# Kernel tuning notes

Measured on AMD Instinct MI355X. Metric: run time of the kernel, lower is better.

## Reference

```python
import jax, jax.numpy as jnp
import numpy as np

B, S, E, N = 2, 2048, 768, 12
H = E // N

def setup_inputs() -> dict:
    key = jax.random.key(0)
    k1, k2, k3, k4, k5 = jax.random.split(key, 5)
    x = jax.random.normal(k1, (B, S, E), dtype=jnp.float32)
    Wqkv = jax.random.normal(k2, (E, 3 * E), dtype=jnp.float32) * (1.0 / np.sqrt(E))
    bqkv = jax.random.normal(k3, (3 * E,), dtype=jnp.float32) * 0.02
    Wproj = jax.random.normal(k4, (E, E), dtype=jnp.float32) * (1.0 / np.sqrt(E))
    bproj = jax.random.normal(k5, (E,), dtype=jnp.float32) * 0.02
    mask = jnp.tril(jnp.ones((S, S), dtype=jnp.int32))[None, None]  # (1,1,S,S) causal
    return {"mask": mask, "x": x, "Wqkv": Wqkv, "bqkv": bqkv, "Wproj": Wproj, "bproj": bproj}

def reference(mask, x, Wqkv, bqkv, Wproj, bproj):
    Bx, Sx, Ex = x.shape
    Hd = Ex // N
    qkv = x @ Wqkv + bqkv                       # (B,S,3E)
    q, k, v = jnp.split(qkv, 3, axis=-1)
    q = q.reshape(Bx, Sx, N, Hd).transpose(0, 2, 1, 3)  # (B,N,S,H)
    k = k.reshape(Bx, Sx, N, Hd).transpose(0, 2, 1, 3)
    v = v.reshape(Bx, Sx, N, Hd).transpose(0, 2, 1, 3)
    att = jnp.einsum('bnsh,bnth->bnst', q, k) / jnp.sqrt(jnp.float32(Hd))
    att = jnp.where(mask == 0, -jnp.inf, att)   # causal masked_fill
    p = jax.nn.softmax(att, axis=-1)            # dropout p=0.0 -> identity
    y = jnp.einsum('bnst,bnth->bnsh', p, v)     # (B,N,S,H)
    y = y.transpose(0, 2, 1, 3).reshape(Bx, Sx, Ex)
    return y @ Wproj + bproj
```

## Files before the change

kernel.cpp:

```cpp
#include <hip/hip_runtime.h>
#include <hip/hip_bf16.h>
#include <math.h>

#define S_LEN 2048
#define E_DIM 768
#define NHEAD 12
#define HDIM 64
#define BATCH 2
#define MROWS (BATCH * S_LEN)
#define KDIM E_DIM
#define NBN (BATCH * NHEAD)
#define NTASKS 768

#define QSCALE 0.1803368801111204f
#define REF2   11.541560327111707f

typedef __attribute__((ext_vector_type(8))) short bf16x8;
typedef __attribute__((ext_vector_type(4))) float f32x4;

__device__ inline float exp2_fast(float x) {
    return __builtin_amdgcn_exp2f(x);
}

__device__ inline unsigned short f2bf(float f) {
    __hip_bfloat16 h = __float2bfloat16(f);
    union { __hip_bfloat16 b; unsigned short u; } v; v.b = h;
    return v.u;
}

__global__ __launch_bounds__(256) void prep(
    const float* __restrict__ x, unsigned short* __restrict__ Xb,
    const float* __restrict__ Wqkv, unsigned short* __restrict__ WqkvT,
    const float* __restrict__ Wproj, unsigned short* __restrict__ WprojT)
{
    __shared__ float t[32][33];
    const int blk = blockIdx.x, tid = threadIdx.x;
    if (blk < 3072) {
        const int i = blk * 256 + tid;
        const float4 a = ((const float4*)x)[i];
        ushort4 o;
        o.x = f2bf(a.x); o.y = f2bf(a.y); o.z = f2bf(a.z); o.w = f2bf(a.w);
        ((ushort4*)Xb)[i] = o;
        return;
    }
    const float* W; unsigned short* WT; int N, bt;
    if (blk < 3072 + 1728) { bt = blk - 3072; N = 3 * E_DIM; W = Wqkv; WT = WqkvT; }
    else                   { bt = blk - 4800; N = E_DIM;     W = Wproj; WT = WprojT; }
    const int bx = bt % (N / 32), by = bt / (N / 32);
    const int k0 = by * 32, n0 = bx * 32;
    const int r = tid >> 3, c4 = (tid & 7) * 4;
    const float4 v = *(const float4*)&W[(size_t)(k0 + r) * N + n0 + c4];
    t[r][c4 + 0] = v.x; t[r][c4 + 1] = v.y; t[r][c4 + 2] = v.z; t[r][c4 + 3] = v.w;
    __syncthreads();
    ushort4 o;
    o.x = f2bf(t[c4 + 0][r]); o.y = f2bf(t[c4 + 1][r]);
    o.z = f2bf(t[c4 + 2][r]); o.w = f2bf(t[c4 + 3][r]);
    *(ushort4*)&WT[(size_t)(n0 + r) * KDIM + k0 + c4] = o;
}

template <int EPI, int BM, int BN>
__global__ __launch_bounds__(256, 3) void gemm_t(
    const unsigned short* __restrict__ A, const unsigned short* __restrict__ BT,
    const float* __restrict__ bias, void* __restrict__ out0,
    void* __restrict__ out1, void* __restrict__ out2, int Nn)
{
    constexpr int MF = BM / 32;
    constexpr int NF = BN / 32;
    __shared__ unsigned short As[BM * 64];
    __shared__ unsigned short Bs[BN * 64];
    const int tid = threadIdx.x;
    const int lane = tid & 63;
    const int wid = tid >> 6;
    const int lr = lane & 15, lg = lane >> 4;
    const int wr = wid >> 1, wc = wid & 1;
    const int m0 = blockIdx.y * BM;
    const int n0 = blockIdx.x * BN;
    const int srow = lane >> 3, scol = (lane & 7) * 8;

    f32x4 acc[MF][NF];
    #pragma unroll
    for (int i = 0; i < MF; ++i)
        #pragma unroll
        for (int j = 0; j < NF; ++j) acc[i][j] = (f32x4){0.f, 0.f, 0.f, 0.f};

    for (int k0 = 0; k0 < KDIM; k0 += 64) {
        __syncthreads();
        #pragma unroll
        for (int c = 0; c < MF; ++c) {
            const int chunk = wid * MF + c;
            const int row = chunk * 8 + srow;
            const unsigned short* ga = A + (size_t)(m0 + row) * KDIM + k0 + scol;
            __builtin_amdgcn_global_load_lds(
                (const __attribute__((address_space(1))) void*)ga,
                (__attribute__((address_space(3))) void*)&As[chunk * 512], 16, 0, 0);
        }
        #pragma unroll
        for (int c = 0; c < NF; ++c) {
            const int chunk = wid * NF + c;
            const int row = chunk * 8 + srow;
            const unsigned short* gb = BT + (size_t)(n0 + row) * KDIM + k0 + scol;
            __builtin_amdgcn_global_load_lds(
                (const __attribute__((address_space(1))) void*)gb,
                (__attribute__((address_space(3))) void*)&Bs[chunk * 512], 16, 0, 0);
        }
        __syncthreads();

        #pragma unroll
        for (int kk = 0; kk < 2; ++kk) {
            bf16x8 af[MF], bf[NF];
            #pragma unroll
            for (int mt = 0; mt < MF; ++mt)
                af[mt] = *(const bf16x8*)&As[(wr * (BM / 2) + mt * 16 + lr) * 64 + kk * 32 + lg * 8];
            #pragma unroll
            for (int nt = 0; nt < NF; ++nt)
                bf[nt] = *(const bf16x8*)&Bs[(wc * (BN / 2) + nt * 16 + lr) * 64 + kk * 32 + lg * 8];
            #pragma unroll
            for (int mt = 0; mt < MF; ++mt)
                #pragma unroll
                for (int nt = 0; nt < NF; ++nt)
                    acc[mt][nt] = __builtin_amdgcn_mfma_f32_16x16x32_bf16(
                        af[mt], bf[nt], acc[mt][nt], 0, 0, 0);
        }
    }

    #pragma unroll
    for (int mt = 0; mt < MF; ++mt) {
        const int rowbase = m0 + wr * (BM / 2) + mt * 16 + lg * 4;
        #pragma unroll
        for (int nt = 0; nt < NF; ++nt) {
            const int col = n0 + wc * (BN / 2) + nt * 16 + lr;
            if (EPI == 0) {
                float* O = (float*)out0;
                const float bv = bias[col];
                #pragma unroll
                for (int r = 0; r < 4; ++r)
                    O[(size_t)(rowbase + r) * Nn + col] = acc[mt][nt][r] + bv;
            } else {
                const int which = col / E_DIM;
                const int rem = col % E_DIM;
                const int head = rem >> 6, h = rem & 63;
                const float bv = bias[col];
                if (which == 2) {
                    const int b = rowbase >> 11, s0 = rowbase & (S_LEN - 1);
                    const int scolv = (s0 & ~63) | ((s0 & 63) ^ ((h & 7) << 3));
                    unsigned short* VT = (unsigned short*)out2;
                    ushort4 pk;
                    pk.x = f2bf(acc[mt][nt][0] + bv);
                    pk.y = f2bf(acc[mt][nt][1] + bv);
                    pk.z = f2bf(acc[mt][nt][2] + bv);
                    pk.w = f2bf(acc[mt][nt][3] + bv);
                    *(ushort4*)&VT[((size_t)(b * NHEAD + head) * HDIM + h) * S_LEN + scolv] = pk;
                } else {
                    unsigned short* dst = (which == 0) ? (unsigned short*)out0
                                                       : (unsigned short*)out1;
                    const float sc = (which == 0) ? QSCALE : 1.0f;
                    #pragma unroll
                    for (int r = 0; r < 4; ++r) {
                        const int m = rowbase + r;
                        const int b = m >> 11, s = m & (S_LEN - 1);
                        const int hh = (which == 1) ? (h ^ ((s & 7) << 3)) : h;
                        dst[(((size_t)(b * NHEAD + head) * S_LEN) + s) * HDIM + hh] =
                            f2bf((acc[mt][nt][r] + bv) * sc);
                    }
                }
            }
        }
    }
}

__global__ __launch_bounds__(256, 4) void attn_mfma(
    const unsigned short* __restrict__ Qb, const unsigned short* __restrict__ Kb,
    const unsigned short* __restrict__ VTb, unsigned short* __restrict__ Y,
    float* __restrict__ ws_o, float* __restrict__ ws_l)
{
    __shared__ unsigned short smem[5 * 4096];

    const int tid = threadIdx.x;
    const int lane = tid & 63;
    const int wid = tid >> 6;
    const int lr = lane & 15;
    const int lg = lane >> 4;

    unsigned short* const Pw = smem + 16384 + wid * 1024;

    const short one_bf = (short)0x3F80;
    bf16x8 onesB;
    #pragma unroll
    for (int j = 0; j < 8; ++j) onesB[j] = one_bf;

    const int B = blockIdx.x;
    const int xcd = B & 7, slot = B >> 3;
    const int bn = xcd + (slot >> 5) * 8;
    const int rest = slot & 31;
    const int jj = rest & 15, half = rest >> 4;
    const int b = bn / NHEAD, n = bn % NHEAD;

    const unsigned short* Kg = Kb + (size_t)bn * S_LEN * HDIM;
    const unsigned short* Vg = VTb + (size_t)bn * HDIM * S_LEN;

    auto run_pass = [&](int qb, int t0, int t1, int mode) {
        const size_t qoff = ((size_t)bn * S_LEN + (qb * 64 + wid * 16 + lr)) * HDIM;
        const bf16x8 qB0 = *(const bf16x8*)(Qb + qoff + lg * 8);
        const bf16x8 qB1 = *(const bf16x8*)(Qb + qoff + 32 + lg * 8);

        f32x4 o[4];
        #pragma unroll
        for (int ht = 0; ht < 4; ++ht) o[ht] = (f32x4){0.f, 0.f, 0.f, 0.f};
        f32x4 lsum = (f32x4){0.f, 0.f, 0.f, 0.f};

        __syncthreads();
        #pragma unroll
        for (int e = 0; e < 2; ++e) {
            const int chunk = wid * 2 + e;
            __builtin_amdgcn_global_load_lds(
                (const __attribute__((address_space(1))) void*)
                    (Kg + (size_t)t0 * 4096 + chunk * 512 + lane * 8),
                (__attribute__((address_space(3))) void*)&smem[chunk * 512], 16, 0, 0);
            __builtin_amdgcn_global_load_lds(
                (const __attribute__((address_space(1))) void*)
                    (Vg + (size_t)(chunk * 8 + (lane >> 3)) * S_LEN + t0 * 64 + (lane & 7) * 8),
                (__attribute__((address_space(3))) void*)&smem[8192 + chunk * 512], 16, 0, 0);
        }

        int cur = 0;
        for (int t = t0; t < t1; ++t) {
            __syncthreads();
            if (t + 1 < t1) {
                #pragma unroll
                for (int e = 0; e < 2; ++e) {
                    const int chunk = wid * 2 + e;
                    __builtin_amdgcn_global_load_lds(
                        (const __attribute__((address_space(1))) void*)
                            (Kg + (size_t)(t + 1) * 4096 + chunk * 512 + lane * 8),
                        (__attribute__((address_space(3))) void*)
                            &smem[(cur ^ 1) * 4096 + chunk * 512], 16, 0, 0);
                    __builtin_amdgcn_global_load_lds(
                        (const __attribute__((address_space(1))) void*)
                            (Vg + (size_t)(chunk * 8 + (lane >> 3)) * S_LEN + (t + 1) * 64
                                + (lane & 7) * 8),
                        (__attribute__((address_space(3))) void*)
                            &smem[8192 + (cur ^ 1) * 4096 + chunk * 512], 16, 0, 0);
                }
            }

            const unsigned short* Kc = smem + cur * 4096;
            const unsigned short* Vc = smem + 8192 + cur * 4096;

            f32x4 s[4];
            __builtin_amdgcn_s_setprio(1);
            #pragma unroll
            for (int ct = 0; ct < 4; ++ct) {
                const int kr = ct * 16 + lr;
                const int xo = (kr & 7) << 3;
                const bf16x8 kb0 = *(const bf16x8*)&Kc[kr * 64 + ((lg * 8) ^ xo)];
                const bf16x8 kb1 = *(const bf16x8*)&Kc[kr * 64 + ((32 + lg * 8) ^ xo)];
                f32x4 a = (f32x4){0.f, 0.f, 0.f, 0.f};
                a = __builtin_amdgcn_mfma_f32_16x16x32_bf16(kb0, qB0, a, 0, 0, 0);
                a = __builtin_amdgcn_mfma_f32_16x16x32_bf16(kb1, qB1, a, 0, 0, 0);
                s[ct] = a;
            }
            __builtin_amdgcn_s_setprio(0);

            if (t == qb) {
                const int q = qb * 64 + wid * 16 + lr;
                #pragma unroll
                for (int ct = 0; ct < 4; ++ct) {
                    #pragma unroll
                    for (int r = 0; r < 4; ++r) {
                        const int k = t * 64 + ct * 16 + lg * 4 + r;
                        if (k > q) s[ct][r] = -1e30f;
                    }
                }
            }

            const int pxo = (lr & 7) << 3;
            #pragma unroll
            for (int ct = 0; ct < 4; ++ct) {
                const float p0 = exp2_fast(s[ct][0] - REF2);
                const float p1 = exp2_fast(s[ct][1] - REF2);
                const float p2 = exp2_fast(s[ct][2] - REF2);
                const float p3 = exp2_fast(s[ct][3] - REF2);
                ushort4 pk;
                pk.x = f2bf(p0); pk.y = f2bf(p1); pk.z = f2bf(p2); pk.w = f2bf(p3);
                *(ushort4*)&Pw[lr * 64 + ((ct * 16 + lg * 4) ^ pxo)] = pk;
            }

            const bf16x8 pa0 = *(const bf16x8*)&Pw[lr * 64 + ((lg * 8) ^ pxo)];
            const bf16x8 pa1 = *(const bf16x8*)&Pw[lr * 64 + ((32 + lg * 8) ^ pxo)];
            __builtin_amdgcn_s_setprio(1);
            lsum = __builtin_amdgcn_mfma_f32_16x16x32_bf16(pa0, onesB, lsum, 0, 0, 0);
            lsum = __builtin_amdgcn_mfma_f32_16x16x32_bf16(pa1, onesB, lsum, 0, 0, 0);
            #pragma unroll
            for (int ht = 0; ht < 4; ++ht) {
                const int h = ht * 16 + lr;
                const int xo = (h & 7) << 3;
                const bf16x8 vb0 = *(const bf16x8*)&Vc[h * 64 + ((lg * 8) ^ xo)];
                const bf16x8 vb1 = *(const bf16x8*)&Vc[h * 64 + ((32 + lg * 8) ^ xo)];
                o[ht] = __builtin_amdgcn_mfma_f32_16x16x32_bf16(pa0, vb0, o[ht], 0, 0, 0);
                o[ht] = __builtin_amdgcn_mfma_f32_16x16x32_bf16(pa1, vb1, o[ht], 0, 0, 0);
            }
            __builtin_amdgcn_s_setprio(0);
            cur ^= 1;
        }

        if (mode == 2) {
            float invl[4];
            #pragma unroll
            for (int r = 0; r < 4; ++r) invl[r] = 1.f / lsum[r];
            #pragma unroll
            for (int r = 0; r < 4; ++r) {
                const int qrow = qb * 64 + wid * 16 + lg * 4 + r;
                unsigned short* yrow =
                    Y + ((size_t)(b * S_LEN + qrow)) * E_DIM + n * HDIM;
                #pragma unroll
                for (int ht = 0; ht < 4; ++ht)
                    yrow[ht * 16 + lr] = f2bf(o[ht][r] * invl[r]);
            }
        } else {
            const size_t m = (size_t)(bn * 16 + (qb - 16)) * 2 + mode;
            float* wo = ws_o + m * 4096;
            const int rowl = wid * 16 + lg * 4;
            #pragma unroll
            for (int ht = 0; ht < 4; ++ht)
                #pragma unroll
                for (int r = 0; r < 4; ++r)
                    wo[(rowl + r) * 64 + ht * 16 + lr] = o[ht][r];
            if (lr == 0) {
                #pragma unroll
                for (int r = 0; r < 4; ++r)
                    ws_l[m * 64 + rowl + r] = lsum[r];
            }
        }
    };

    if (half == 0) {
        run_pass(31 - jj, 0, 16, 0);
    } else {
        run_pass(31 - jj, 16, 32 - jj, 1);
        run_pass(jj, 0, jj + 1, 2);
    }
}

__global__ __launch_bounds__(256) void attn_merge(
    const float* __restrict__ ws_o, const float* __restrict__ ws_l,
    unsigned short* __restrict__ Y)
{
    const int m = blockIdx.x;
    const int bn = m / 16, qb = 16 + (m % 16);
    const int b = bn / NHEAD, n = bn % NHEAD;
    const int tid = threadIdx.x;
    const int r = tid >> 2, h0 = (tid & 3) * 16;

    const float* o0 = ws_o + ((size_t)m * 2 + 0) * 4096 + r * 64 + h0;
    const float* o1 = ws_o + ((size_t)m * 2 + 1) * 4096 + r * 64 + h0;
    const float l = ws_l[((size_t)m * 2 + 0) * 64 + r] +
                    ws_l[((size_t)m * 2 + 1) * 64 + r];
    const float inv = 1.f / l;
    unsigned short* yrow =
        Y + ((size_t)(b * S_LEN + qb * 64 + r)) * E_DIM + n * HDIM + h0;
    #pragma unroll
    for (int q = 0; q < 16; q += 4) {
        const float4 a = *(const float4*)(o0 + q);
        const float4 c = *(const float4*)(o1 + q);
        ushort4 pk;
        pk.x = f2bf((a.x + c.x) * inv); pk.y = f2bf((a.y + c.y) * inv);
        pk.z = f2bf((a.z + c.z) * inv); pk.w = f2bf((a.w + c.w) * inv);
        *(ushort4*)&yrow[q] = pk;
    }
}

extern "C" void kernel_launch(void* const* d_in, const int* in_sizes, int n_in,
                              void* d_out, int out_size, void* d_ws, size_t ws_size,
                              hipStream_t stream) {
    const float* x     = (const float*)d_in[1];
    const float* Wqkv  = (const float*)d_in[2];
    const float* bqkv  = (const float*)d_in[3];
    const float* Wproj = (const float*)d_in[4];
    const float* bproj = (const float*)d_in[5];
    float* out = (float*)d_out;

    const size_t per = (size_t)BATCH * NHEAD * S_LEN * HDIM;
    unsigned short* Xb     = (unsigned short*)d_ws;
    unsigned short* WqkvT  = Xb + (size_t)MROWS * E_DIM;
    unsigned short* WprojT = WqkvT + (size_t)3 * E_DIM * E_DIM;
    unsigned short* Qb     = WprojT + (size_t)E_DIM * E_DIM;
    unsigned short* Kb     = Qb + per;
    unsigned short* VTb    = Kb + per;
    unsigned short* Yb     = VTb + per;
    float*          ws_o   = (float*)(Yb + (size_t)MROWS * E_DIM);
    float*          ws_l   = ws_o + (size_t)384 * 2 * 4096;

    prep<<<5376, 256, 0, stream>>>(x, Xb, Wqkv, WqkvT, Wproj, WprojT);
    gemm_t<1, 128, 96><<<dim3(3 * E_DIM / 96, MROWS / 128), 256, 0, stream>>>(
        Xb, WqkvT, bqkv, Qb, Kb, VTb, 3 * E_DIM);
    attn_mfma<<<NTASKS, 256, 0, stream>>>(Qb, Kb, VTb, Yb, ws_o, ws_l);
    attn_merge<<<384, 256, 0, stream>>>(ws_o, ws_l, Yb);
    gemm_t<0, 64, 64><<<dim3(E_DIM / 64, MROWS / 64), 256, 0, stream>>>(
        Yb, WprojT, bproj, out, nullptr, nullptr, E_DIM);
}
```

Baseline: 78.61 us.

## Double-buffer GEMM LDS staging with K=32 tiles; store split-attention partials in bf16

The GEMM mainloop now uses two LDS buffers with 32-wide K tiles. The next tile's global-to-LDS load is issued before computing on the current one, and one barrier per iteration is dropped. The hope is to overlap memory latency with MFMA work, at the cost of twice as many loop iterations with half the work each. Separately, the split-attention partial outputs are stored as bf16 instead of fp32, which halves workspace traffic for the merge kernel at some accuracy cost.

After: 82.23 us. 1.05x slower.

```diff
diff --git a/kernel.cpp b/kernel.cpp
--- a/kernel.cpp
+++ b/kernel.cpp
@@ -26,6 +26,11 @@
     __hip_bfloat16 h = __float2bfloat16(f);
     union { __hip_bfloat16 b; unsigned short u; } v; v.b = h;
     return v.u;
+}
+
+__device__ inline float bf2f(unsigned short u) {
+    union { unsigned u32; float f; } v; v.u32 = ((unsigned)u) << 16;
+    return v.f;
 }
 
 __global__ __launch_bounds__(256) void prep(
@@ -66,8 +71,10 @@
 {
     constexpr int MF = BM / 32;
     constexpr int NF = BN / 32;
-    __shared__ unsigned short As[BM * 64];
-    __shared__ unsigned short Bs[BN * 64];
+    constexpr int ACH = BM / 16;
+    constexpr int BCH = BN / 16;
+    __shared__ unsigned short As[2][BM * 32];
+    __shared__ unsigned short Bs[2][BN * 32];
     const int tid = threadIdx.x;
     const int lane = tid & 63;
     const int wid = tid >> 6;
@@ -75,7 +82,7 @@
     const int wr = wid >> 1, wc = wid & 1;
     const int m0 = blockIdx.y * BM;
     const int n0 = blockIdx.x * BN;
-    const int srow = lane >> 3, scol = (lane & 7) * 8;
+    const int crow = lane >> 2, ccol = (lane & 3) * 8;
 
     f32x4 acc[MF][NF];
     #pragma unroll
@@ -83,44 +90,47 @@
         #pragma unroll
         for (int j = 0; j < NF; ++j) acc[i][j] = (f32x4){0.f, 0.f, 0.f, 0.f};
 
-    for (int k0 = 0; k0 < KDIM; k0 += 64) {
+    auto stage = [&](int buf, int k0) {
+        for (int c = wid; c < ACH + BCH; c += 4) {
+            if (c < ACH) {
+                const unsigned short* g =
+                    A + (size_t)(m0 + c * 16 + crow) * KDIM + k0 + ccol;
+                __builtin_amdgcn_global_load_lds(
+                    (const __attribute__((address_space(1))) void*)g,
+                    (__attribute__((address_space(3))) void*)&As[buf][c * 512],
+                    16, 0, 0);
+            } else {
+                const int cb = c - ACH;
+                const unsigned short* g =
+                    BT + (size_t)(n0 + cb * 16 + crow) * KDIM + k0 + ccol;
+                __builtin_amdgcn_global_load_lds(
+                    (const __attribute__((address_space(1))) void*)g,
+                    (__attribute__((address_space(3))) void*)&Bs[buf][cb * 512],
+                    16, 0, 0);
+            }
+        }
+    };
+
+    stage(0, 0);
+    int cur = 0;
+    constexpr int NT = KDIM / 32;
+    for (int t = 0; t < NT; ++t) {
         __syncthreads();
-        #pragma unroll
-        for (int c = 0; c < MF; ++c) {
-            const int chunk = wid * MF + c;
-            const int row = chunk * 8 + srow;
-            const unsigned short* ga = A + (size_t)(m0 + row) * KDIM + k0 + scol;
-            __builtin_amdgcn_global_load_lds(
-                (const __attribute__((address_space(1))) void*)ga,
-                (__attribute__((address_space(3))) void*)&As[chunk * 512], 16, 0, 0);
-        }
-        #pragma unroll
-        for (int c = 0; c < NF; ++c) {
-            const int chunk = wid * NF + c;
-            const int row = chunk * 8 + srow;
-            const unsigned short* gb = BT + (size_t)(n0 + row) * KDIM + k0 + scol;
-            __builtin_amdgcn_global_load_lds(
-                (const __attribute__((address_space(1))) void*)gb,
-                (__attribute__((address_space(3))) void*)&Bs[chunk * 512], 16, 0, 0);
-        }
-        __syncthreads();
-
-        #pragma unroll
-        for (int kk = 0; kk < 2; ++kk) {
-            bf16x8 af[MF], bf[NF];
-            #pragma unroll
-            for (int mt = 0; mt < MF; ++mt)
-                af[mt] = *(const bf16x8*)&As[(wr * (BM / 2) + mt * 16 + lr) * 64 + kk * 32 + lg * 8];
+        if (t + 1 < NT) stage(cur ^ 1, (t + 1) * 32);
+        bf16x8 af[MF], bf[NF];
+        #pragma unroll
+        for (int mt = 0; mt < MF; ++mt)
+            af[mt] = *(const bf16x8*)&As[cur][(wr * (BM / 2) + mt * 16 + lr) * 32 + lg * 8];
+        #pragma unroll
+        for (int nt = 0; nt < NF; ++nt)
+            bf[nt] = *(const bf16x8*)&Bs[cur][(wc * (BN / 2) + nt * 16 + lr) * 32 + lg * 8];
+        #pragma unroll
+        for (int mt = 0; mt < MF; ++mt)
             #pragma unroll
             for (int nt = 0; nt < NF; ++nt)
-                bf[nt] = *(const bf16x8*)&Bs[(wc * (BN / 2) + nt * 16 + lr) * 64 + kk * 32 + lg * 8];
-            #pragma unroll
-            for (int mt = 0; mt < MF; ++mt)
-                #pragma unroll
-                for (int nt = 0; nt < NF; ++nt)
-                    acc[mt][nt] = __builtin_amdgcn_mfma_f32_16x16x32_bf16(
-                        af[mt], bf[nt], acc[mt][nt], 0, 0, 0);
-        }
+                acc[mt][nt] = __builtin_amdgcn_mfma_f32_16x16x32_bf16(
+                    af[mt], bf[nt], acc[mt][nt], 0, 0, 0);
+        cur ^= 1;
     }
 
     #pragma unroll
@@ -171,7 +181,7 @@
 __global__ __launch_bounds__(256, 4) void attn_mfma(
     const unsigned short* __restrict__ Qb, const unsigned short* __restrict__ Kb,
     const unsigned short* __restrict__ VTb, unsigned short* __restrict__ Y,
-    float* __restrict__ ws_o, float* __restrict__ ws_l)
+    unsigned short* __restrict__ ws_o, float* __restrict__ ws_l)
 {
     __shared__ unsigned short smem[5 * 4096];
 
@@ -318,13 +328,13 @@
             }
         } else {
             const size_t m = (size_t)(bn * 16 + (qb - 16)) * 2 + mode;
-            float* wo = ws_o + m * 4096;
+            unsigned short* wo = ws_o + m * 4096;
             const int rowl = wid * 16 + lg * 4;
             #pragma unroll
             for (int ht = 0; ht < 4; ++ht)
                 #pragma unroll
                 for (int r = 0; r < 4; ++r)
-                    wo[(rowl + r) * 64 + ht * 16 + lr] = o[ht][r];
+                    wo[(rowl + r) * 64 + ht * 16 + lr] = f2bf(o[ht][r]);
             if (lr == 0) {
                 #pragma unroll
                 for (int r = 0; r < 4; ++r)
@@ -342,7 +352,7 @@
 }
 
 __global__ __launch_bounds__(256) void attn_merge(
-    const float* __restrict__ ws_o, const float* __restrict__ ws_l,
+    const unsigned short* __restrict__ ws_o, const float* __restrict__ ws_l,
     unsigned short* __restrict__ Y)
 {
     const int m = blockIdx.x;
@@ -351,8 +361,8 @@
     const int tid = threadIdx.x;
     const int r = tid >> 2, h0 = (tid & 3) * 16;
 
-    const float* o0 = ws_o + ((size_t)m * 2 + 0) * 4096 + r * 64 + h0;
-    const float* o1 = ws_o + ((size_t)m * 2 + 1) * 4096 + r * 64 + h0;
+    const unsigned short* o0 = ws_o + ((size_t)m * 2 + 0) * 4096 + r * 64 + h0;
+    const unsigned short* o1 = ws_o + ((size_t)m * 2 + 1) * 4096 + r * 64 + h0;
     const float l = ws_l[((size_t)m * 2 + 0) * 64 + r] +
                     ws_l[((size_t)m * 2 + 1) * 64 + r];
     const float inv = 1.f / l;
@@ -360,11 +370,13 @@
         Y + ((size_t)(b * S_LEN + qb * 64 + r)) * E_DIM + n * HDIM + h0;
     #pragma unroll
     for (int q = 0; q < 16; q += 4) {
-        const float4 a = *(const float4*)(o0 + q);
-        const float4 c = *(const float4*)(o1 + q);
+        const ushort4 a = *(const ushort4*)(o0 + q);
+        const ushort4 c = *(const ushort4*)(o1 + q);
         ushort4 pk;
-        pk.x = f2bf((a.x + c.x) * inv); pk.y = f2bf((a.y + c.y) * inv);
-        pk.z = f2bf((a.z + c.z) * inv); pk.w = f2bf((a.w + c.w) * inv);
+        pk.x = f2bf((bf2f(a.x) + bf2f(c.x)) * inv);
+        pk.y = f2bf((bf2f(a.y) + bf2f(c.y)) * inv);
+        pk.z = f2bf((bf2f(a.z) + bf2f(c.z)) * inv);
+        pk.w = f2bf((bf2f(a.w) + bf2f(c.w)) * inv);
         *(ushort4*)&yrow[q] = pk;
     }
 }
@@ -387,8 +399,8 @@
     unsigned short* Kb     = Qb + per;
     unsigned short* VTb    = Kb + per;
     unsigned short* Yb     = VTb + per;
-    float*          ws_o   = (float*)(Yb + (size_t)MROWS * E_DIM);
-    float*          ws_l   = ws_o + (size_t)384 * 2 * 4096;
+    unsigned short* ws_o   = Yb + (size_t)MROWS * E_DIM;
+    float*          ws_l   = (float*)(ws_o + (size_t)384 * 2 * 4096);
 
     prep<<<5376, 256, 0, stream>>>(x, Xb, Wqkv, WqkvT, Wproj, WprojT);
     gemm_t<1, 128, 96><<<dim3(3 * E_DIM / 96, MROWS / 128), 256, 0, stream>>>(
```
